# Kernel tuning notes

Hardware: AMD Instinct MI355X
Metric: run time of the kernel (lower is better)

The kernel has to match this reference:

```python
import jax, jax.numpy as jnp
import numpy as np

N, E, D, CAT, BINS, B, NNEG = 50000, 1600000, 128, 768, 100, 4096, 4


def _spmm(row, col, val, x):
    # torch.spmm(adj, x) with adj in COO form: out[r] += val * x[c]
    return jax.ops.segment_sum(val[:, None] * x[col], row, num_segments=N)


def _bn(x, g, b):
    # BatchNorm1d in training mode: biased batch statistics
    m = jnp.mean(x, axis=0)
    v = jnp.var(x, axis=0)
    return (x - m) * jax.lax.rsqrt(v + 1e-5) * g + b


def _two_att(qx, x, Wq1, bq1, Wk1, bk1, Wv1, bv1, Wq2, bq2, Wk2, bk2, Wv2, bv2, Wcat, bcat):
    # qx, x: [b, 2, D]. NOTE: original uses nn.Softmax(dim=1), i.e. softmax over the
    # QUERY axis of the [b, q, k] score matrix -- reproduced faithfully here.
    scale = 1.0 / (D ** 0.5)
    q = qx @ Wq1 + bq1
    k = x @ Wk1 + bk1
    v = x @ Wv1 + bv1
    a = jax.nn.softmax(jnp.einsum('bqd,bkd->bqk', q, k) * scale, axis=1)
    h = jnp.einsum('bqk,bkd->bqd', a, v)
    q = h @ Wq2 + bq2
    k = h @ Wk2 + bk2
    v = h @ Wv2 + bv2
    a = jax.nn.softmax(jnp.einsum('bqd,bkd->bqk', q, k) * scale, axis=1)
    h = jnp.einsum('bqk,bkd->bqd', a, v)
    return jnp.concatenate([h[:, 0], h[:, 1]], axis=1) @ Wcat + bcat


def setup_inputs():
    key = jax.random.key(0)
    ks = jax.random.split(key, 32)
    p = lambda i, shape: jax.random.normal(ks[i], shape, dtype=jnp.float32) * 0.05
    return {
        'features': jax.random.normal(ks[0], (N, 2 * CAT), dtype=jnp.float32),
        'price': jax.random.randint(ks[1], (N,), 0, BINS),
        'adj_row': jax.random.randint(ks[2], (E,), 0, N),
        'adj_col': jax.random.randint(ks[3], (E,), 0, N),
        'adj_val': jax.random.uniform(ks[4], (E,), dtype=jnp.float32),
        'train_set': jax.random.randint(ks[5], (B, 2 + NNEG), 0, N),
        'W_cid2': p(6, (CAT, D)), 'b_cid2': p(7, (D,)),
        'W_cid3': p(8, (CAT, D)), 'b_cid3': p(9, (D,)),
        'price_table': p(10, (BINS, D)),
        'W_emb': p(11, (3 * D, D)), 'b_emb': p(12, (D,)),
        'W_low': p(13, (D, D)), 'W_mid': p(14, (D, D)),
        'bn1_g': jnp.ones((D,), jnp.float32), 'bn1_b': jnp.zeros((D,), jnp.float32),
        'bn2_g': jnp.ones((D,), jnp.float32), 'bn2_b': jnp.zeros((D,), jnp.float32),
        'Wq1': p(15, (D, D)), 'bq1': p(16, (D,)),
        'Wk1': p(17, (D, D)), 'bk1': p(18, (D,)),
        'Wv1': p(19, (D, D)), 'bv1': p(20, (D,)),
        'Wq2': p(21, (D, D)), 'bq2': p(22, (D,)),
        'Wk2': p(23, (D, D)), 'bk2': p(24, (D,)),
        'Wv2': p(25, (D, D)), 'bv2': p(26, (D,)),
        'Wcat': p(27, (2 * D, D)), 'bcat': p(28, (D,)),
    }


def reference(features, price, adj_row, adj_col, adj_val, train_set,
              W_cid2, b_cid2, W_cid3, b_cid3, price_table, W_emb, b_emb,
              W_low, W_mid, bn1_g, bn1_b, bn2_g, bn2_b,
              Wq1, bq1, Wk1, bk1, Wv1, bv1, Wq2, bq2, Wk2, bk2, Wv2, bv2, Wcat, bcat):
    # item embedding
    e2 = features[:, :CAT] @ W_cid2 + b_cid2
    e3 = features[:, CAT:] @ W_cid3 + b_cid3
    ep = price_table[price]
    item = jax.nn.relu(jnp.concatenate([e2, e3, ep], axis=1) @ W_emb + b_emb)  # [N, D]
    # graph convolutions (low / mid frequency)
    ag = _spmm(adj_row, adj_col, adj_val, item)
    low = (0.5 * ag + 0.5 * item) @ W_low
    mid = (0.5 * _spmm(adj_row, adj_col, adj_val, ag) - 0.5 * item) @ W_mid
    out = jnp.stack([_bn(low, bn1_g, bn1_b), _bn(mid, bn2_g, bn2_b)], axis=1)  # [N, 2, D]
    # gather triples
    key_e = out[train_set[:, 0]]   # [B, 2, D]
    pos_e = out[train_set[:, 1]]   # [B, 2, D]
    neg_e = out[train_set[:, 2:]]  # [B, NNEG, 2, D]
    ap = (Wq1, bq1, Wk1, bk1, Wv1, bv1, Wq2, bq2, Wk2, bk2, Wv2, bv2, Wcat, bcat)
    klp = _two_att(pos_e, key_e, *ap)  # [B, D]
    pl = _two_att(key_e, pos_e, *ap)   # [B, D]
    # vectorize the per-negative loop by folding NNEG into batch
    Bn = key_e.shape[0]
    key_rep = jnp.broadcast_to(key_e[:, None], (Bn, NNEG, 2, D)).reshape(Bn * NNEG, 2, D)
    neg_flat = neg_e.reshape(Bn * NNEG, 2, D)
    kln = _two_att(neg_flat, key_rep, *ap).reshape(Bn, NNEG, D)
    nl = _two_att(key_rep, neg_flat, *ap).reshape(Bn, NNEG, D)
    pos_scores = jnp.sum(klp * pl, axis=1)        # [B]
    neg_scores = jnp.sum(kln * nl, axis=2)        # [B, NNEG]
    return -jnp.mean(jnp.log(jax.nn.sigmoid(pos_scores[:, None] - neg_scores) + 1e-9))
```

## Files before the change

kernel.cpp:

```cpp
#include <hip/hip_runtime.h>
#include <hip/hip_bf16.h>


typedef __attribute__((ext_vector_type(4))) float  f32x4;
typedef __attribute__((ext_vector_type(2))) float  f32x2;
typedef __attribute__((ext_vector_type(8))) short  s16x8;
typedef __attribute__((ext_vector_type(4))) short  s16x4;
typedef __attribute__((ext_vector_type(8))) __bf16 bf16x8;

#define NN   50000
#define EE   1600000
#define BQ   4096
#define NNEG 4

__device__ __forceinline__ short f2b(float x) {
    union { float f; unsigned u; } c; c.f = x;
    unsigned r = c.u + 0x7FFF + ((c.u >> 16) & 1);
    return (short)(r >> 16);
}

template<bool TWOSRC, bool PRICE, bool RELU>
__global__ __launch_bounds__(256)
void gemm_bf16(const float* __restrict__ A1, const float* __restrict__ A2,
               float alpha, float beta,
               const short* __restrict__ WT, const float* __restrict__ bias,
               const int* __restrict__ price, const float* __restrict__ ptab,
               float* __restrict__ Y, int ldY, int rows, int K)
{
    __shared__ short Alds[128][32];
    __shared__ short Wlds[128][32];

    const int t    = threadIdx.x;
    const int lane = t & 63;
    const int w    = t >> 6;
    const int r0   = blockIdx.x * 128;
    const int c0   = blockIdx.y * 128;
    const short* WTb = WT + (size_t)c0 * K;

    f32x4 acc[4][4];
#pragma unroll
    for (int m = 0; m < 4; ++m)
#pragma unroll
        for (int n = 0; n < 4; ++n) acc[m][n] = (f32x4)0.f;

    const int srow = t >> 3;
    const int skk  = (t & 7) * 4;
    const int wn   = t >> 1;
    const int wkp  = (t & 1) * 16;

    const int wr   = (w >> 1) * 64;
    const int wc   = (w & 1) * 64;
    const int rsel = lane & 15;
    const int kb   = (lane >> 4) * 8;

    for (int k0 = 0; k0 < K; k0 += 32) {
#pragma unroll
        for (int i = 0; i < 4; ++i) {
            int r  = srow + i * 32;
            int rg = r0 + r; rg = rg < rows ? rg : rows - 1;
            float4 va = *(const float4*)(A1 + (size_t)rg * K + (k0 + skk));
            if (TWOSRC) {
                float4 vb = *(const float4*)(A2 + (size_t)rg * K + (k0 + skk));
                va.x = alpha * va.x + beta * vb.x;
                va.y = alpha * va.y + beta * vb.y;
                va.z = alpha * va.z + beta * vb.z;
                va.w = alpha * va.w + beta * vb.w;
            }
            s16x4 sv; sv[0]=f2b(va.x); sv[1]=f2b(va.y); sv[2]=f2b(va.z); sv[3]=f2b(va.w);
            int sw = ((r >> 1) & 3) * 8;
            *(s16x4*)&Alds[r][skk ^ sw] = sv;
        }
        {
            const short* p = WTb + (size_t)wn * K + (k0 + wkp);
            s16x8 w0 = *(const s16x8*)p;
            s16x8 w1 = *(const s16x8*)(p + 8);
            int sw = ((wn >> 1) & 3) * 8;
            *(s16x8*)&Wlds[wn][wkp ^ sw]       = w0;
            *(s16x8*)&Wlds[wn][(wkp + 8) ^ sw] = w1;
        }
        __syncthreads();

        s16x8 af[4], bfr[4];
#pragma unroll
        for (int m = 0; m < 4; ++m) {
            int r = wr + m * 16 + rsel;
            af[m] = *(const s16x8*)&Alds[r][kb ^ (((r >> 1) & 3) * 8)];
        }
#pragma unroll
        for (int n = 0; n < 4; ++n) {
            int r = wc + n * 16 + rsel;
            bfr[n] = *(const s16x8*)&Wlds[r][kb ^ (((r >> 1) & 3) * 8)];
        }
#pragma unroll
        for (int m = 0; m < 4; ++m)
#pragma unroll
            for (int n = 0; n < 4; ++n)
                acc[m][n] = __builtin_amdgcn_mfma_f32_16x16x32_bf16(
                    __builtin_bit_cast(bf16x8, af[m]),
                    __builtin_bit_cast(bf16x8, bfr[n]), acc[m][n], 0, 0, 0);
        __syncthreads();
    }

    const int crow = (lane >> 4) * 4;
#pragma unroll
    for (int m = 0; m < 4; ++m) {
        int rbase = r0 + wr + m * 16 + crow;
#pragma unroll
        for (int i = 0; i < 4; ++i) {
            int gr = rbase + i;
            bool ok = (gr < rows);
            int pidx = 0;
            if (PRICE) pidx = ok ? price[gr] : 0;
#pragma unroll
            for (int n = 0; n < 4; ++n) {
                int coll = wc + n * 16 + rsel;
                int cc   = c0 + coll;
                float v  = acc[m][n][i];
                if (bias)  v += bias[cc];
                if (PRICE) v += ptab[pidx * 128 + coll];
                if (RELU)  v = fmaxf(v, 0.f);
                if (ok) Y[(size_t)gr * ldY + cc] = v;
            }
        }
    }
}

__global__ __launch_bounds__(256)
void hist_rows(const int* __restrict__ row, int* __restrict__ cnt)
{
    int e = blockIdx.x * 256 + threadIdx.x;
    if (e < EE) atomicAdd(&cnt[row[e]], 1);
}

__global__ __launch_bounds__(1024)
void scan_a(const int* __restrict__ cnt, int* __restrict__ rp, int* __restrict__ bsum)
{
    __shared__ int tmp[1024];
    int t = threadIdx.x, g = blockIdx.x * 1024 + t;
    int v = (g < NN) ? cnt[g] : 0;
    tmp[t] = v;
    __syncthreads();
    for (int off = 1; off < 1024; off <<= 1) {
        int a = (t >= off) ? tmp[t - off] : 0;
        __syncthreads();
        tmp[t] += a;
        __syncthreads();
    }
    if (g < NN) rp[g] = tmp[t] - v;
    if (t == 1023) bsum[blockIdx.x] = tmp[t];
}

__global__ void scan_b(int* __restrict__ bsum, int nb)
{
    if (threadIdx.x == 0) {
        int acc = 0;
        for (int i = 0; i < nb; ++i) { int v = bsum[i]; bsum[i] = acc; acc += v; }
    }
}

__global__ __launch_bounds__(1024)
void scan_c(int* __restrict__ rp, int* __restrict__ cur, const int* __restrict__ bsum)
{
    int t = threadIdx.x, g = blockIdx.x * 1024 + t;
    if (g < NN) {
        int v = rp[g] + bsum[blockIdx.x];
        rp[g] = v; cur[g] = v;
    }
    if (g == 0) rp[NN] = EE;
}

__global__ __launch_bounds__(256)
void scatter_edges(const int* __restrict__ row, const int* __restrict__ col,
                   const float* __restrict__ val, int* __restrict__ cur,
                   int* __restrict__ pcol, float* __restrict__ pval)
{
    int e = blockIdx.x * 256 + threadIdx.x;
    if (e >= EE) return;
    int p = atomicAdd(&cur[row[e]], 1);
    pcol[p] = col[e];
    pval[p] = val[e];
}

__global__ __launch_bounds__(256)
void spmm_csr(const int* __restrict__ rp, const int* __restrict__ pcol,
              const float* __restrict__ pval, const float* __restrict__ x,
              float* __restrict__ y)
{
    int w    = (blockIdx.x * 256 + threadIdx.x) >> 6;
    int lane = threadIdx.x & 63;
    if (w >= NN) return;
    int s = rp[w], e = rp[w + 1];
    int d = lane * 2;
    float ax = 0.f, ay = 0.f;
    int i = s;
    for (; i + 2 <= e; i += 2) {
        int   c0 = pcol[i],   c1 = pcol[i + 1];
        float v0 = pval[i],   v1 = pval[i + 1];
        f32x2 x0 = *(const f32x2*)(x + (size_t)c0 * 128 + d);
        f32x2 x1 = *(const f32x2*)(x + (size_t)c1 * 128 + d);
        ax += v0 * x0.x + v1 * x1.x;
        ay += v0 * x0.y + v1 * x1.y;
    }
    if (i < e) {
        int c0 = pcol[i]; float v0 = pval[i];
        f32x2 x0 = *(const f32x2*)(x + (size_t)c0 * 128 + d);
        ax += v0 * x0.x; ay += v0 * x0.y;
    }
    f32x2 r; r.x = ax; r.y = ay;
    *(f32x2*)(y + (size_t)w * 128 + d) = r;
}

__global__ __launch_bounds__(256)
void colstats(const float* __restrict__ low, const float* __restrict__ mid,
              float* __restrict__ stats, int nrows)
{
    const float* src = blockIdx.y ? mid : low;
    int c = threadIdx.x & 127;
    int h = threadIdx.x >> 7;
    int rs = blockIdx.x * 512;
    int re = min(rs + 512, nrows);
    float s1 = 0.f, s2 = 0.f;
    for (int r = rs + h; r < re; r += 2) {
        float xv = src[(size_t)r * 128 + c];
        s1 += xv; s2 += xv * xv;
    }
    __shared__ float l1[256], l2[256];
    l1[threadIdx.x] = s1; l2[threadIdx.x] = s2;
    __syncthreads();
    if (h == 0) {
        s1 = l1[c] + l1[128 + c];
        s2 = l2[c] + l2[128 + c];
        atomicAdd(&stats[blockIdx.y * 256 + c],       s1);
        atomicAdd(&stats[blockIdx.y * 256 + 128 + c], s2);
    }
}

__global__ __launch_bounds__(256)
void bn_scalebias(const float* __restrict__ stats,
                  const float* g1, const float* b1,
                  const float* g2, const float* b2,
                  float* __restrict__ sb, float inv_n)
{
    int t = threadIdx.x;
    int mat = t >> 7, c = t & 127;
    float mean = stats[mat * 256 + c] * inv_n;
    float var  = stats[mat * 256 + 128 + c] * inv_n - mean * mean;
    float s = (mat ? g2[c] : g1[c]) * rsqrtf(var + 1e-5f);
    float tt = (mat ? b2[c] : b1[c]) - mean * s;
    sb[mat * 256 + c] = s;
    sb[mat * 256 + 128 + c] = tt;
}

__global__ __launch_bounds__(256)
void gather_norm(const float* __restrict__ low, const float* __restrict__ mid,
                 const float* __restrict__ sb, const int* __restrict__ ts,
                 float* __restrict__ out, int nb, int slot0, int nslots)
{
    int idx = blockIdx.x * 256 + threadIdx.x;
    if (idx >= nb * nslots * 256) return;
    int c   = idx & 127;
    int seq = (idx >> 7) & 1;
    int r   = idx >> 8;
    int b = r / nslots, j = r - b * nslots;
    int node = ts[b * 6 + slot0 + j];
    const float* src = seq ? mid : low;
    float xv = src[(size_t)node * 128 + c];
    out[(size_t)r * 256 + seq * 128 + c] = xv * sb[seq * 256 + c] + sb[seq * 256 + 128 + c];
}

__global__ __launch_bounds__(256)
void attn_kernel(const float* __restrict__ qbase, const float* __restrict__ kvbase,
                 float* __restrict__ h, int nb, int qshift, int kvshift)
{
    int gw   = (blockIdx.x * 256 + threadIdx.x) >> 6;
    int lane = threadIdx.x & 63;
    if (gw >= nb) return;
    int qb = (gw >> qshift) * 2;
    int kb = (gw >> kvshift) * 2;
    const float* q0 = qbase + (size_t)qb * 384;
    const float* q1 = q0 + 384;
    const float* k0 = kvbase + (size_t)kb * 384 + 128;
    const float* k1 = k0 + 384;
    const float* v0 = kvbase + (size_t)kb * 384 + 256;
    const float* v1 = v0 + 384;
    int d = lane * 2;
    f32x2 q0v = *(const f32x2*)(q0 + d);
    f32x2 q1v = *(const f32x2*)(q1 + d);
    f32x2 k0v = *(const f32x2*)(k0 + d);
    f32x2 k1v = *(const f32x2*)(k1 + d);
    float s00 = q0v.x*k0v.x + q0v.y*k0v.y;
    float s01 = q0v.x*k1v.x + q0v.y*k1v.y;
    float s10 = q1v.x*k0v.x + q1v.y*k0v.y;
    float s11 = q1v.x*k1v.x + q1v.y*k1v.y;
#pragma unroll
    for (int off = 32; off; off >>= 1) {
        s00 += __shfl_xor(s00, off);
        s01 += __shfl_xor(s01, off);
        s10 += __shfl_xor(s10, off);
        s11 += __shfl_xor(s11, off);
    }
    const float scale = 0.08838834764831845f;
    s00 *= scale; s01 *= scale; s10 *= scale; s11 *= scale;
    float m0 = fmaxf(s00, s10), m1 = fmaxf(s01, s11);
    float e00 = __expf(s00 - m0), e10 = __expf(s10 - m0);
    float e01 = __expf(s01 - m1), e11 = __expf(s11 - m1);
    float i0 = 1.f / (e00 + e10), i1 = 1.f / (e01 + e11);
    float a00 = e00 * i0, a10 = e10 * i0;
    float a01 = e01 * i1, a11 = e11 * i1;
    f32x2 v0v = *(const f32x2*)(v0 + d);
    f32x2 v1v = *(const f32x2*)(v1 + d);
    f32x2 h0, h1;
    h0.x = a00*v0v.x + a01*v1v.x;  h0.y = a00*v0v.y + a01*v1v.y;
    h1.x = a10*v0v.x + a11*v1v.x;  h1.y = a10*v0v.y + a11*v1v.y;
    *(f32x2*)(h + (size_t)(gw * 2)     * 128 + d) = h0;
    *(f32x2*)(h + (size_t)(gw * 2 + 1) * 128 + d) = h1;
}

__global__ __launch_bounds__(256)
void scores_kernel(const float* __restrict__ cat, float* __restrict__ scores)
{
    int gw   = (blockIdx.x * 256 + threadIdx.x) >> 6;
    int lane = threadIdx.x & 63;
    if (gw >= 20480) return;
    const float *pa, *pb;
    if (gw < BQ) { pa = cat + (size_t)gw * 128;            pb = cat + (size_t)(BQ + gw) * 128; }
    else { int n = gw - BQ; pa = cat + (size_t)(2*BQ + n) * 128; pb = cat + (size_t)(2*BQ + BQ*NNEG + n) * 128; }
    f32x2 a = *(const f32x2*)(pa + lane * 2);
    f32x2 b = *(const f32x2*)(pb + lane * 2);
    float s = a.x * b.x + a.y * b.y;
#pragma unroll
    for (int off = 32; off; off >>= 1) s += __shfl_xor(s, off);
    if (lane == 0) scores[gw] = s;
}

__global__ __launch_bounds__(256)
void loss_kernel(const float* __restrict__ scores, float* __restrict__ out)
{
    int t = threadIdx.x;
    float acc = 0.f;
    for (int i = t; i < BQ * NNEG; i += 256) {
        int b = i >> 2;
        float x = scores[b] - scores[BQ + i];
        float sig = 1.f / (1.f + __expf(-x));
        acc += __logf(sig + 1e-9f);
    }
    __shared__ float red[256];
    red[t] = acc; __syncthreads();
    for (int s = 128; s > 0; s >>= 1) { if (t < s) red[t] += red[t + s]; __syncthreads(); }
    if (t == 0) out[0] = -red[0] / (float)(BQ * NNEG);
}

__global__ void pack_wc(const float* __restrict__ W2, const float* __restrict__ W3,
                        const float* __restrict__ We, short* __restrict__ WcT)
{
    int k = blockIdx.x, n = threadIdx.x;
    const float* Wrow = (k < 768) ? (W2 + (size_t)k * 128) : (W3 + (size_t)(k - 768) * 128);
    const float* Web  = We + ((k < 768) ? 0 : 128 * 128);
    float acc = 0.f;
    for (int j = 0; j < 128; ++j) acc += Wrow[j] * Web[j * 128 + n];
    WcT[(size_t)n * 1536 + k] = f2b(acc);
}

__global__ void pack_ptab(const float* __restrict__ PT, const float* __restrict__ We,
                          float* __restrict__ ptab2)
{
    int p = blockIdx.x, n = threadIdx.x;
    const float* Web = We + 256 * 128;
    float acc = 0.f;
    for (int j = 0; j < 128; ++j) acc += PT[p * 128 + j] * Web[j * 128 + n];
    ptab2[p * 128 + n] = acc;
}

__global__ void pack_biasc(const float* b2, const float* b3, const float* bemb,
                           const float* __restrict__ We, float* __restrict__ bias_c)
{
    int n = threadIdx.x;
    float acc = bemb[n];
    for (int j = 0; j < 128; ++j)
        acc += b2[j] * We[j * 128 + n] + b3[j] * We[(128 + j) * 128 + n];
    bias_c[n] = acc;
}

__global__ void pack_wt(const float* __restrict__ W, short* __restrict__ WT, int K)
{
    int k = blockIdx.x, n = threadIdx.x;
    WT[(size_t)n * K + k] = f2b(W[(size_t)k * 128 + n]);
}

__global__ void pack_wt3(const float* Wq, const float* Wk, const float* Wv,
                         const float* bq, const float* bk, const float* bv,
                         short* __restrict__ WT, float* __restrict__ bout)
{
    int k = blockIdx.x, n = threadIdx.x;
    const float* W = (n < 128) ? Wq : ((n < 256) ? Wk : Wv);
    int nl = n & 127;
    WT[(size_t)n * 128 + k] = f2b(W[k * 128 + nl]);
    if (k == 0) {
        const float* b = (n < 128) ? bq : ((n < 256) ? bk : bv);
        bout[n] = b[nl];
    }
}

extern "C" void kernel_launch(void* const* d_in, const int* in_sizes, int n_in,
                              void* d_out, int out_size, void* d_ws, size_t ws_size,
                              hipStream_t stream)
{
    const float* features = (const float*)d_in[0];
    const int*   price    = (const int*)  d_in[1];
    const int*   adj_row  = (const int*)  d_in[2];
    const int*   adj_col  = (const int*)  d_in[3];
    const float* adj_val  = (const float*)d_in[4];
    const int*   train_set= (const int*)  d_in[5];
    const float* W_cid2   = (const float*)d_in[6];
    const float* b_cid2   = (const float*)d_in[7];
    const float* W_cid3   = (const float*)d_in[8];
    const float* b_cid3   = (const float*)d_in[9];
    const float* ptable   = (const float*)d_in[10];
    const float* W_emb    = (const float*)d_in[11];
    const float* b_emb    = (const float*)d_in[12];
    const float* W_low    = (const float*)d_in[13];
    const float* W_mid    = (const float*)d_in[14];
    const float* bn1_g    = (const float*)d_in[15];
    const float* bn1_b    = (const float*)d_in[16];
    const float* bn2_g    = (const float*)d_in[17];
    const float* bn2_b    = (const float*)d_in[18];
    const float* Wq1 = (const float*)d_in[19]; const float* bq1 = (const float*)d_in[20];
    const float* Wk1 = (const float*)d_in[21]; const float* bk1 = (const float*)d_in[22];
    const float* Wv1 = (const float*)d_in[23]; const float* bv1 = (const float*)d_in[24];
    const float* Wq2 = (const float*)d_in[25]; const float* bq2 = (const float*)d_in[26];
    const float* Wk2 = (const float*)d_in[27]; const float* bk2 = (const float*)d_in[28];
    const float* Wv2 = (const float*)d_in[29]; const float* bv2 = (const float*)d_in[30];
    const float* Wcat= (const float*)d_in[31]; const float* bcat= (const float*)d_in[32];

    float* ws = (float*)d_ws;

    const size_t SZ_NODE  = (size_t)NN * 128;
    const size_t OFF_ITEM = 0;
    const size_t OFF_AG   = SZ_NODE;
    const size_t OFF_AG2  = 2 * SZ_NODE;
    const size_t OFF_LOW  = 3 * SZ_NODE;
    const size_t OFF_MID  = 4 * SZ_NODE;
    const size_t OFF_QKV2 = 0;
    const size_t OFF_GATH = 5 * SZ_NODE;
    const size_t OFF_H2   = OFF_GATH;
    const size_t OFF_QKV1 = OFF_GATH + 6291456;
    const size_t OFF_H1   = OFF_QKV1 + 18874368;
    const size_t OFF_CAT  = OFF_H1;
    size_t o = OFF_H1 + 10485760;
    short* WcT    = (short*)(ws + o);  o += 98304;
    float* ptab2  = ws + o;            o += 12800;
    float* bias_c = ws + o;            o += 128;
    short* Wqkv1T = (short*)(ws + o);  o += 24576;
    float* bqkv1  = ws + o;            o += 384;
    short* Wqkv2T = (short*)(ws + o);  o += 24576;
    float* bqkv2  = ws + o;            o += 384;
    short* WlowT  = (short*)(ws + o);  o += 8192;
    short* WmidT  = (short*)(ws + o);  o += 8192;
    short* WcatT  = (short*)(ws + o);  o += 16384;
    float* stats  = ws + o;            o += 512;
    float* sb     = ws + o;            o += 512;
    float* scores = ws + o;            o += 20480;

    float* item = ws + OFF_ITEM;
    float* ag   = ws + OFF_AG;
    float* ag2  = ws + OFF_AG2;
    float* low  = ws + OFF_LOW;
    float* mid  = ws + OFF_MID;
    float* gath = ws + OFF_GATH;
    float* qkv1 = ws + OFF_QKV1;
    float* h1   = ws + OFF_H1;
    float* qkv2 = ws + OFF_QKV2;
    float* h2   = ws + OFF_H2;
    float* cat  = ws + OFF_CAT;

    int*   rp   = (int*)(ws + OFF_GATH);
    int*   cur  = rp + 50008;
    int*   bsum = cur + 50008;
    int*   pcol = bsum + 64 + 56;
    float* pval = (float*)(pcol + 1600000);

    hipLaunchKernelGGL(pack_wc,   dim3(1536), dim3(128), 0, stream, W_cid2, W_cid3, W_emb, WcT);
    hipLaunchKernelGGL(pack_ptab, dim3(100),  dim3(128), 0, stream, ptable, W_emb, ptab2);
    hipLaunchKernelGGL(pack_biasc,dim3(1),    dim3(128), 0, stream, b_cid2, b_cid3, b_emb, W_emb, bias_c);
    hipLaunchKernelGGL(pack_wt3,  dim3(128),  dim3(384), 0, stream, Wq1, Wk1, Wv1, bq1, bk1, bv1, Wqkv1T, bqkv1);
    hipLaunchKernelGGL(pack_wt3,  dim3(128),  dim3(384), 0, stream, Wq2, Wk2, Wv2, bq2, bk2, bv2, Wqkv2T, bqkv2);
    hipLaunchKernelGGL(pack_wt,   dim3(128),  dim3(128), 0, stream, W_low, WlowT, 128);
    hipLaunchKernelGGL(pack_wt,   dim3(128),  dim3(128), 0, stream, W_mid, WmidT, 128);
    hipLaunchKernelGGL(pack_wt,   dim3(256),  dim3(128), 0, stream, Wcat,  WcatT, 256);

    hipMemsetAsync(stats, 0, 512 * sizeof(float), stream);
    hipMemsetAsync(cur, 0, 50000 * sizeof(int), stream);

    hipLaunchKernelGGL(hist_rows,     dim3(6250), dim3(256),  0, stream, adj_row, cur);
    hipLaunchKernelGGL(scan_a,        dim3(49),   dim3(1024), 0, stream, cur, rp, bsum);
    hipLaunchKernelGGL(scan_b,        dim3(1),    dim3(64),   0, stream, bsum, 49);
    hipLaunchKernelGGL(scan_c,        dim3(49),   dim3(1024), 0, stream, rp, cur, bsum);
    hipLaunchKernelGGL(scatter_edges, dim3(6250), dim3(256),  0, stream,
                       adj_row, adj_col, adj_val, cur, pcol, pval);

    hipLaunchKernelGGL((gemm_bf16<false, true, true>), dim3(391, 1), dim3(256), 0, stream,
                       features, nullptr, 1.f, 0.f, WcT, bias_c, price, ptab2,
                       item, 128, NN, 1536);

    hipLaunchKernelGGL(spmm_csr, dim3(12500), dim3(256), 0, stream, rp, pcol, pval, item, ag);
    hipLaunchKernelGGL((gemm_bf16<true, false, false>), dim3(391, 1), dim3(256), 0, stream,
                       ag, item, 0.5f, 0.5f, WlowT, nullptr, nullptr, nullptr,
                       low, 128, NN, 128);

    hipLaunchKernelGGL(spmm_csr, dim3(12500), dim3(256), 0, stream, rp, pcol, pval, ag, ag2);
    hipLaunchKernelGGL((gemm_bf16<true, false, false>), dim3(391, 1), dim3(256), 0, stream,
                       ag2, item, 0.5f, -0.5f, WmidT, nullptr, nullptr, nullptr,
                       mid, 128, NN, 128);

    hipLaunchKernelGGL(colstats, dim3(98, 2), dim3(256), 0, stream, low, mid, stats, NN);
    hipLaunchKernelGGL(bn_scalebias, dim3(1), dim3(256), 0, stream,
                       stats, bn1_g, bn1_b, bn2_g, bn2_b, sb, 1.f / (float)NN);

    hipLaunchKernelGGL(gather_norm, dim3(4096),  dim3(256), 0, stream, low, mid, sb, train_set, gath,              BQ, 0, 1);
    hipLaunchKernelGGL(gather_norm, dim3(4096),  dim3(256), 0, stream, low, mid, sb, train_set, gath + 8192*128,   BQ, 1, 1);
    hipLaunchKernelGGL(gather_norm, dim3(16384), dim3(256), 0, stream, low, mid, sb, train_set, gath + 16384*128,  BQ, 2, 4);

    hipLaunchKernelGGL((gemm_bf16<false, false, false>), dim3(384, 3), dim3(256), 0, stream,
                       gath, nullptr, 1.f, 0.f, Wqkv1T, bqkv1, nullptr, nullptr,
                       qkv1, 384, 49152, 128);

    hipLaunchKernelGGL(attn_kernel, dim3(1024), dim3(256), 0, stream,
                       qkv1 + (size_t)8192*384, qkv1, h1, BQ, 0, 0);
    hipLaunchKernelGGL(attn_kernel, dim3(1024), dim3(256), 0, stream,
                       qkv1, qkv1 + (size_t)8192*384, h1 + (size_t)8192*128, BQ, 0, 0);
    hipLaunchKernelGGL(attn_kernel, dim3(4096), dim3(256), 0, stream,
                       qkv1 + (size_t)16384*384, qkv1, h1 + (size_t)16384*128, BQ*NNEG, 0, 2);
    hipLaunchKernelGGL(attn_kernel, dim3(4096), dim3(256), 0, stream,
                       qkv1, qkv1 + (size_t)16384*384, h1 + (size_t)49152*128, BQ*NNEG, 2, 0);

    hipLaunchKernelGGL((gemm_bf16<false, false, false>), dim3(640, 3), dim3(256), 0, stream,
                       h1, nullptr, 1.f, 0.f, Wqkv2T, bqkv2, nullptr, nullptr,
                       qkv2, 384, 81920, 128);

    const size_t rb[4] = { 0, 8192, 16384, 49152 };
    const int    nbs[4] = { BQ, BQ, BQ*NNEG, BQ*NNEG };
    for (int f = 0; f < 4; ++f) {
        hipLaunchKernelGGL(attn_kernel, dim3((nbs[f] + 3) / 4), dim3(256), 0, stream,
                           qkv2 + rb[f]*384, qkv2 + rb[f]*384, h2 + rb[f]*128, nbs[f], 0, 0);
    }

    hipLaunchKernelGGL((gemm_bf16<false, false, false>), dim3(320, 1), dim3(256), 0, stream,
                       h2, nullptr, 1.f, 0.f, WcatT, bcat, nullptr, nullptr,
                       cat, 128, 40960, 256);

    hipLaunchKernelGGL(scores_kernel, dim3(5120), dim3(256), 0, stream, cat, scores);
    hipLaunchKernelGGL(loss_kernel, dim3(1), dim3(256), 0, stream, scores, (float*)d_out);
}
```

Before: 1.293 ms.

## Store intermediates in bf16 and merge attention, gather and pack launches

SpMM gathers now read bf16 copies of the node features, and the CSR column and value arrays are interleaved into a single int2 array. The attention-stage buffers (gathered rows, qkv, h) are stored as bf16, and a new GEMM variant loads bf16 A tiles directly. The separate attention, gather and weight-pack launches are merged into single kernels, and scan_b uses a wave shuffle scan. This cuts memory traffic and launch count, at the cost of extra bf16 rounding on activations and SpMM inputs.

```diff
diff --git a/kernel.cpp b/kernel.cpp
--- a/kernel.cpp
+++ b/kernel.cpp
@@ -18,14 +18,20 @@
     unsigned r = c.u + 0x7FFF + ((c.u >> 16) & 1);
     return (short)(r >> 16);
 }
-
-template<bool TWOSRC, bool PRICE, bool RELU>
+__device__ __forceinline__ float blo(unsigned u) { return __builtin_bit_cast(float, u << 16); }
+__device__ __forceinline__ float bhi(unsigned u) { return __builtin_bit_cast(float, u & 0xffff0000u); }
+__device__ __forceinline__ unsigned pk2(float a, float b) {
+    return (unsigned)(unsigned short)f2b(a) | ((unsigned)(unsigned short)f2b(b) << 16);
+}
+
+template<bool TWOSRC, bool PRICE, bool RELU, bool OUTBF>
 __global__ __launch_bounds__(256)
 void gemm_bf16(const float* __restrict__ A1, const float* __restrict__ A2,
                float alpha, float beta,
                const short* __restrict__ WT, const float* __restrict__ bias,
                const int* __restrict__ price, const float* __restrict__ ptab,
-               float* __restrict__ Y, int ldY, int rows, int K)
+               float* __restrict__ Y, unsigned short* __restrict__ Yb,
+               int ldY, int rows, int K)
 {
     __shared__ short Alds[128][32];
     __shared__ short Wlds[128][32];
@@ -119,7 +125,106 @@
                 if (bias)  v += bias[cc];
                 if (PRICE) v += ptab[pidx * 128 + coll];
                 if (RELU)  v = fmaxf(v, 0.f);
-                if (ok) Y[(size_t)gr * ldY + cc] = v;
+                if (ok) {
+                    Y[(size_t)gr * ldY + cc] = v;
+                    if (OUTBF) Yb[(size_t)gr * ldY + cc] = (unsigned short)f2b(v);
+                }
+            }
+        }
+    }
+}
+
+template<bool OUTBF>
+__global__ __launch_bounds__(256)
+void gemm_a16(const unsigned short* __restrict__ A,
+              const short* __restrict__ WT, const float* __restrict__ bias,
+              float* __restrict__ Y, unsigned short* __restrict__ Yb,
+              int ldY, int rows, int K)
+{
+    __shared__ short Alds[128][32];
+    __shared__ short Wlds[128][32];
+
+    const int t    = threadIdx.x;
+    const int lane = t & 63;
+    const int w    = t >> 6;
+    const int r0   = blockIdx.x * 128;
+    const int c0   = blockIdx.y * 128;
+    const short* WTb = WT + (size_t)c0 * K;
+
+    f32x4 acc[4][4];
+#pragma unroll
+    for (int m = 0; m < 4; ++m)
+#pragma unroll
+        for (int n = 0; n < 4; ++n) acc[m][n] = (f32x4)0.f;
+
+    const int srow = t >> 1;
+    const int skk  = (t & 1) * 16;
+    const int wn   = t >> 1;
+    const int wkp  = (t & 1) * 16;
+
+    const int wr   = (w >> 1) * 64;
+    const int wc   = (w & 1) * 64;
+    const int rsel = lane & 15;
+    const int kb   = (lane >> 4) * 8;
+
+    for (int k0 = 0; k0 < K; k0 += 32) {
+        {
+            int rg = r0 + srow; rg = rg < rows ? rg : rows - 1;
+            const unsigned short* p = A + (size_t)rg * K + (k0 + skk);
+            s16x8 a0 = *(const s16x8*)p;
+            s16x8 a1 = *(const s16x8*)(p + 8);
+            int sw = ((srow >> 1) & 3) * 8;
+            *(s16x8*)&Alds[srow][skk ^ sw]       = a0;
+            *(s16x8*)&Alds[srow][(skk + 8) ^ sw] = a1;
+        }
+        {
+            const short* p = WTb + (size_t)wn * K + (k0 + wkp);
+            s16x8 w0 = *(const s16x8*)p;
+            s16x8 w1 = *(const s16x8*)(p + 8);
+            int sw = ((wn >> 1) & 3) * 8;
+            *(s16x8*)&Wlds[wn][wkp ^ sw]       = w0;
+            *(s16x8*)&Wlds[wn][(wkp + 8) ^ sw] = w1;
+        }
+        __syncthreads();
+
+        s16x8 af[4], bfr[4];
+#pragma unroll
+        for (int m = 0; m < 4; ++m) {
+            int r = wr + m * 16 + rsel;
+            af[m] = *(const s16x8*)&Alds[r][kb ^ (((r >> 1) & 3) * 8)];
+        }
+#pragma unroll
+        for (int n = 0; n < 4; ++n) {
+            int r = wc + n * 16 + rsel;
+            bfr[n] = *(const s16x8*)&Wlds[r][kb ^ (((r >> 1) & 3) * 8)];
+        }
+#pragma unroll
+        for (int m = 0; m < 4; ++m)
+#pragma unroll
+            for (int n = 0; n < 4; ++n)
+                acc[m][n] = __builtin_amdgcn_mfma_f32_16x16x32_bf16(
+                    __builtin_bit_cast(bf16x8, af[m]),
+                    __builtin_bit_cast(bf16x8, bfr[n]), acc[m][n], 0, 0, 0);
+        __syncthreads();
+    }
+
+    const int crow = (lane >> 4) * 4;
+#pragma unroll
+    for (int m = 0; m < 4; ++m) {
+        int rbase = r0 + wr + m * 16 + crow;
+#pragma unroll
+        for (int i = 0; i < 4; ++i) {
+            int gr = rbase + i;
+            bool ok = (gr < rows);
+#pragma unroll
+            for (int n = 0; n < 4; ++n) {
+                int cc = c0 + wc + n * 16 + rsel;
+                float v = acc[m][n][i];
+                if (bias) v += bias[cc];
+                if (ok) {
+                    if (OUTBF) Yb[(size_t)gr * ldY + cc] = (unsigned short)f2b(v);
+                    else       Y [(size_t)gr * ldY + cc] = v;
+                }
             }
         }
     }
@@ -150,12 +255,17 @@
     if (t == 1023) bsum[blockIdx.x] = tmp[t];
 }
 
-__global__ void scan_b(int* __restrict__ bsum, int nb)
-{
-    if (threadIdx.x == 0) {
-        int acc = 0;
-        for (int i = 0; i < nb; ++i) { int v = bsum[i]; bsum[i] = acc; acc += v; }
-    }
+__global__ __launch_bounds__(64)
+void scan_b(int* __restrict__ bsum, int nb)
+{
+    int lane = threadIdx.x;
+    int orig = (lane < nb) ? bsum[lane] : 0;
+    int v = orig;
+    for (int off = 1; off < 64; off <<= 1) {
+        int u = __shfl_up(v, off);
+        if (lane >= off) v += u;
+    }
+    if (lane < nb) bsum[lane] = v - orig;
 }
 
 __global__ __launch_bounds__(1024)
@@ -172,19 +282,19 @@
 __global__ __launch_bounds__(256)
 void scatter_edges(const int* __restrict__ row, const int* __restrict__ col,
                    const float* __restrict__ val, int* __restrict__ cur,
-                   int* __restrict__ pcol, float* __restrict__ pval)
+                   int2* __restrict__ pedge)
 {
     int e = blockIdx.x * 256 + threadIdx.x;
     if (e >= EE) return;
     int p = atomicAdd(&cur[row[e]], 1);
-    pcol[p] = col[e];
-    pval[p] = val[e];
-}
-
-__global__ __launch_bounds__(256)
-void spmm_csr(const int* __restrict__ rp, const int* __restrict__ pcol,
-              const float* __restrict__ pval, const float* __restrict__ x,
-              float* __restrict__ y)
+    pedge[p] = make_int2(col[e], __float_as_int(val[e]));
+}
+
+template<bool WRITEB>
+__global__ __launch_bounds__(256)
+void spmm_csr(const int* __restrict__ rp, const int2* __restrict__ pedge,
+              const unsigned short* __restrict__ xb,
+              float* __restrict__ y, unsigned short* __restrict__ yb)
 {
     int w    = (blockIdx.x * 256 + threadIdx.x) >> 6;
     int lane = threadIdx.x & 63;
@@ -193,21 +303,28 @@
     int d = lane * 2;
     float ax = 0.f, ay = 0.f;
     int i = s;
-    for (; i + 2 <= e; i += 2) {
-        int   c0 = pcol[i],   c1 = pcol[i + 1];
-        float v0 = pval[i],   v1 = pval[i + 1];
-        f32x2 x0 = *(const f32x2*)(x + (size_t)c0 * 128 + d);
-        f32x2 x1 = *(const f32x2*)(x + (size_t)c1 * 128 + d);
-        ax += v0 * x0.x + v1 * x1.x;
-        ay += v0 * x0.y + v1 * x1.y;
-    }
-    if (i < e) {
-        int c0 = pcol[i]; float v0 = pval[i];
-        f32x2 x0 = *(const f32x2*)(x + (size_t)c0 * 128 + d);
-        ax += v0 * x0.x; ay += v0 * x0.y;
+    for (; i + 4 <= e; i += 4) {
+        int2 e0 = pedge[i], e1 = pedge[i+1], e2 = pedge[i+2], e3 = pedge[i+3];
+        unsigned x0 = *(const unsigned*)(xb + (size_t)e0.x * 128 + d);
+        unsigned x1 = *(const unsigned*)(xb + (size_t)e1.x * 128 + d);
+        unsigned x2 = *(const unsigned*)(xb + (size_t)e2.x * 128 + d);
+        unsigned x3 = *(const unsigned*)(xb + (size_t)e3.x * 128 + d);
+        float v0 = __builtin_bit_cast(float, e0.y);
+        float v1 = __builtin_bit_cast(float, e1.y);
+        float v2 = __builtin_bit_cast(float, e2.y);
+        float v3 = __builtin_bit_cast(float, e3.y);
+        ax += v0 * blo(x0) + v1 * blo(x1) + v2 * blo(x2) + v3 * blo(x3);
+        ay += v0 * bhi(x0) + v1 * bhi(x1) + v2 * bhi(x2) + v3 * bhi(x3);
+    }
+    for (; i < e; ++i) {
+        int2 e0 = pedge[i];
+        unsigned x0 = *(const unsigned*)(xb + (size_t)e0.x * 128 + d);
+        float v0 = __builtin_bit_cast(float, e0.y);
+        ax += v0 * blo(x0); ay += v0 * bhi(x0);
     }
     f32x2 r; r.x = ax; r.y = ay;
     *(f32x2*)(y + (size_t)w * 128 + d) = r;
+    if (WRITEB) *(unsigned*)(yb + (size_t)w * 128 + d) = pk2(ax, ay);
 }
 
 __global__ __launch_bounds__(256)
@@ -254,44 +371,47 @@
 __global__ __launch_bounds__(256)
 void gather_norm(const float* __restrict__ low, const float* __restrict__ mid,
                  const float* __restrict__ sb, const int* __restrict__ ts,
-                 float* __restrict__ out, int nb, int slot0, int nslots)
+                 unsigned short* __restrict__ out)
 {
     int idx = blockIdx.x * 256 + threadIdx.x;
-    if (idx >= nb * nslots * 256) return;
     int c   = idx & 127;
     int seq = (idx >> 7) & 1;
     int r   = idx >> 8;
-    int b = r / nslots, j = r - b * nslots;
-    int node = ts[b * 6 + slot0 + j];
-    const float* src = seq ? mid : low;
-    float xv = src[(size_t)node * 128 + c];
-    out[(size_t)r * 256 + seq * 128 + c] = xv * sb[seq * 256 + c] + sb[seq * 256 + 128 + c];
-}
-
-__global__ __launch_bounds__(256)
-void attn_kernel(const float* __restrict__ qbase, const float* __restrict__ kvbase,
-                 float* __restrict__ h, int nb, int qshift, int kvshift)
+    int node;
+    if      (r < 4096) node = ts[r * 6];
+    else if (r < 8192) node = ts[(r - 4096) * 6 + 1];
+    else { int rr = r - 8192; node = ts[(rr >> 2) * 6 + 2 + (rr & 3)]; }
+    float xv = (seq ? mid : low)[(size_t)node * 128 + c];
+    float yv = xv * sb[seq * 256 + c] + sb[seq * 256 + 128 + c];
+    out[(size_t)r * 256 + seq * 128 + c] = (unsigned short)f2b(yv);
+}
+
+template<int LAYER>
+__global__ __launch_bounds__(256)
+void attn_fused(const unsigned short* __restrict__ qkv,
+                unsigned short* __restrict__ h, int ntot)
 {
     int gw   = (blockIdx.x * 256 + threadIdx.x) >> 6;
     int lane = threadIdx.x & 63;
-    if (gw >= nb) return;
-    int qb = (gw >> qshift) * 2;
-    int kb = (gw >> kvshift) * 2;
-    const float* q0 = qbase + (size_t)qb * 384;
-    const float* q1 = q0 + 384;
-    const float* k0 = kvbase + (size_t)kb * 384 + 128;
-    const float* k1 = k0 + 384;
-    const float* v0 = kvbase + (size_t)kb * 384 + 256;
-    const float* v1 = v0 + 384;
+    if (gw >= ntot) return;
+    int qtok, ktok, orow;
+    if (LAYER == 1) {
+        if      (gw < 4096)  { int g = gw;         qtok = 8192  + g*2; ktok = g*2;          orow = g*2; }
+        else if (gw < 8192)  { int g = gw - 4096;  qtok = g*2;         ktok = 8192 + g*2;   orow = 8192 + g*2; }
+        else if (gw < 24576) { int g = gw - 8192;  qtok = 16384 + g*2; ktok = (g>>2)*2;     orow = 16384 + g*2; }
+        else                 { int g = gw - 24576; qtok = (g>>2)*2;    ktok = 16384 + g*2;  orow = 49152 + g*2; }
+    } else {
+        qtok = gw * 2; ktok = gw * 2; orow = gw * 2;
+    }
     int d = lane * 2;
-    f32x2 q0v = *(const f32x2*)(q0 + d);
-    f32x2 q1v = *(const f32x2*)(q1 + d);
-    f32x2 k0v = *(const f32x2*)(k0 + d);
-    f32x2 k1v = *(const f32x2*)(k1 + d);
-    float s00 = q0v.x*k0v.x + q0v.y*k0v.y;
-    float s01 = q0v.x*k1v.x + q0v.y*k1v.y;
-    float s10 = q1v.x*k0v.x + q1v.y*k0v.y;
-    float s11 = q1v.x*k1v.x + q1v.y*k1v.y;
+    unsigned q0 = *(const unsigned*)(qkv + (size_t)qtok * 384 + d);
+    unsigned q1 = *(const unsigned*)(qkv + (size_t)(qtok+1) * 384 + d);
+    unsigned k0 = *(const unsigned*)(qkv + (size_t)ktok * 384 + 128 + d);
+    unsigned k1 = *(const unsigned*)(qkv + (size_t)(ktok+1) * 384 + 128 + d);
+    float s00 = blo(q0)*blo(k0) + bhi(q0)*bhi(k0);
+    float s01 = blo(q0)*blo(k1) + bhi(q0)*bhi(k1);
+    float s10 = blo(q1)*blo(k0) + bhi(q1)*bhi(k0);
+    float s11 = blo(q1)*blo(k1) + bhi(q1)*bhi(k1);
 #pragma unroll
     for (int off = 32; off; off >>= 1) {
         s00 += __shfl_xor(s00, off);
@@ -307,13 +427,12 @@
     float i0 = 1.f / (e00 + e10), i1 = 1.f / (e01 + e11);
     float a00 = e00 * i0, a10 = e10 * i0;
     float a01 = e01 * i1, a11 = e11 * i1;
-    f32x2 v0v = *(const f32x2*)(v0 + d);
-    f32x2 v1v = *(const f32x2*)(v1 + d);
-    f32x2 h0, h1;
-    h0.x = a00*v0v.x + a01*v1v.x;  h0.y = a00*v0v.y + a01*v1v.y;
-    h1.x = a10*v0v.x + a11*v1v.x;  h1.y = a10*v0v.y + a11*v1v.y;
-    *(f32x2*)(h + (size_t)(gw * 2)     * 128 + d) = h0;
-    *(f32x2*)(h + (size_t)(gw * 2 + 1) * 128 + d) = h1;
+    unsigned v0 = *(const unsigned*)(qkv + (size_t)ktok * 384 + 256 + d);
+    unsigned v1 = *(const unsigned*)(qkv + (size_t)(ktok+1) * 384 + 256 + d);
+    float h0x = a00*blo(v0) + a01*blo(v1), h0y = a00*bhi(v0) + a01*bhi(v1);
+    float h1x = a10*blo(v0) + a11*blo(v1), h1y = a10*bhi(v0) + a11*bhi(v1);
+    *(unsigned*)(h + (size_t)orow * 128 + d)       = pk2(h0x, h0y);
+    *(unsigned*)(h + (size_t)(orow + 1) * 128 + d) = pk2(h1x, h1y);
 }
 
 __global__ __launch_bounds__(256)
@@ -361,43 +480,51 @@
     WcT[(size_t)n * 1536 + k] = f2b(acc);
 }
 
-__global__ void pack_ptab(const float* __restrict__ PT, const float* __restrict__ We,
-                          float* __restrict__ ptab2)
-{
-    int p = blockIdx.x, n = threadIdx.x;
-    const float* Web = We + 256 * 128;
-    float acc = 0.f;
-    for (int j = 0; j < 128; ++j) acc += PT[p * 128 + j] * Web[j * 128 + n];
-    ptab2[p * 128 + n] = acc;
-}
-
-__global__ void pack_biasc(const float* b2, const float* b3, const float* bemb,
-                           const float* __restrict__ We, float* __restrict__ bias_c)
-{
-    int n = threadIdx.x;
-    float acc = bemb[n];
-    for (int j = 0; j < 128; ++j)
-        acc += b2[j] * We[j * 128 + n] + b3[j] * We[(128 + j) * 128 + n];
-    bias_c[n] = acc;
-}
-
-__global__ void pack_wt(const float* __restrict__ W, short* __restrict__ WT, int K)
-{
-    int k = blockIdx.x, n = threadIdx.x;
-    WT[(size_t)n * K + k] = f2b(W[(size_t)k * 128 + n]);
-}
-
-__global__ void pack_wt3(const float* Wq, const float* Wk, const float* Wv,
-                         const float* bq, const float* bk, const float* bv,
-                         short* __restrict__ WT, float* __restrict__ bout)
-{
-    int k = blockIdx.x, n = threadIdx.x;
-    const float* W = (n < 128) ? Wq : ((n < 256) ? Wk : Wv);
-    int nl = n & 127;
-    WT[(size_t)n * 128 + k] = f2b(W[k * 128 + nl]);
-    if (k == 0) {
-        const float* b = (n < 128) ? bq : ((n < 256) ? bk : bv);
-        bout[n] = b[nl];
+__global__ __launch_bounds__(128)
+void pack_misc(const float* PT, const float* We,
+               const float* b2, const float* b3, const float* bemb,
+               const float* Wq1, const float* Wk1, const float* Wv1,
+               const float* bq1, const float* bk1, const float* bv1,
+               const float* Wq2, const float* Wk2, const float* Wv2,
+               const float* bq2, const float* bk2, const float* bv2,
+               const float* Wlow, const float* Wmid, const float* Wct,
+               float* ptab2, float* bias_c,
+               short* Wqkv1T, float* bqkv1,
+               short* Wqkv2T, float* bqkv2,
+               short* WlowT, short* WmidT, short* WcatT)
+{
+    int b = blockIdx.x, t = threadIdx.x;
+    if (b < 100) {
+        const float* Web = We + 256 * 128;
+        float acc = 0.f;
+        for (int j = 0; j < 128; ++j) acc += PT[b * 128 + j] * Web[j * 128 + t];
+        ptab2[b * 128 + t] = acc;
+    } else if (b == 100) {
+        float acc = bemb[t];
+        for (int j = 0; j < 128; ++j)
+            acc += b2[j] * We[j * 128 + t] + b3[j] * We[(128 + j) * 128 + t];
+        bias_c[t] = acc;
+    } else if (b < 229) {
+        int k = b - 101;
+        Wqkv1T[(size_t)(      t) * 128 + k] = f2b(Wq1[k * 128 + t]);
+        Wqkv1T[(size_t)(128 + t) * 128 + k] = f2b(Wk1[k * 128 + t]);
+        Wqkv1T[(size_t)(256 + t) * 128 + k] = f2b(Wv1[k * 128 + t]);
+        if (k == 0) { bqkv1[t] = bq1[t]; bqkv1[128 + t] = bk1[t]; bqkv1[256 + t] = bv1[t]; }
+    } else if (b < 357) {
+        int k = b - 229;
+        Wqkv2T[(size_t)(      t) * 128 + k] = f2b(Wq2[k * 128 + t]);
+        Wqkv2T[(size_t)(128 + t) * 128 + k] = f2b(Wk2[k * 128 + t]);
+        Wqkv2T[(size_t)(256 + t) * 128 + k] = f2b(Wv2[k * 128 + t]);
+        if (k == 0) { bqkv2[t] = bq2[t]; bqkv2[128 + t] = bk2[t]; bqkv2[256 + t] = bv2[t]; }
+    } else if (b < 485) {
+        int k = b - 357;
+        WlowT[(size_t)t * 128 + k] = f2b(Wlow[k * 128 + t]);
+    } else if (b < 613) {
+        int k = b - 485;
+        WmidT[(size_t)t * 128 + k] = f2b(Wmid[k * 128 + t]);
+    } else {
+        int k = b - 613;
+        WcatT[(size_t)t * 256 + k] = f2b(Wct[k * 128 + t]);
     }
 }
 
@@ -434,119 +561,93 @@
 
     float* ws = (float*)d_ws;
 
-    const size_t SZ_NODE  = (size_t)NN * 128;
-    const size_t OFF_ITEM = 0;
-    const size_t OFF_AG   = SZ_NODE;
-    const size_t OFF_AG2  = 2 * SZ_NODE;
-    const size_t OFF_LOW  = 3 * SZ_NODE;
-    const size_t OFF_MID  = 4 * SZ_NODE;
-    const size_t OFF_QKV2 = 0;
-    const size_t OFF_GATH = 5 * SZ_NODE;
-    const size_t OFF_H2   = OFF_GATH;
-    const size_t OFF_QKV1 = OFF_GATH + 6291456;
-    const size_t OFF_H1   = OFF_QKV1 + 18874368;
-    const size_t OFF_CAT  = OFF_H1;
-    size_t o = OFF_H1 + 10485760;
-    short* WcT    = (short*)(ws + o);  o += 98304;
-    float* ptab2  = ws + o;            o += 12800;
-    float* bias_c = ws + o;            o += 128;
-    short* Wqkv1T = (short*)(ws + o);  o += 24576;
-    float* bqkv1  = ws + o;            o += 384;
-    short* Wqkv2T = (short*)(ws + o);  o += 24576;
-    float* bqkv2  = ws + o;            o += 384;
-    short* WlowT  = (short*)(ws + o);  o += 8192;
-    short* WmidT  = (short*)(ws + o);  o += 8192;
-    short* WcatT  = (short*)(ws + o);  o += 16384;
-    float* stats  = ws + o;            o += 512;
-    float* sb     = ws + o;            o += 512;
-    float* scores = ws + o;            o += 20480;
-
-    float* item = ws + OFF_ITEM;
-    float* ag   = ws + OFF_AG;
-    float* ag2  = ws + OFF_AG2;
-    float* low  = ws + OFF_LOW;
-    float* mid  = ws + OFF_MID;
-    float* gath = ws + OFF_GATH;
-    float* qkv1 = ws + OFF_QKV1;
-    float* h1   = ws + OFF_H1;
-    float* qkv2 = ws + OFF_QKV2;
-    float* h2   = ws + OFF_H2;
-    float* cat  = ws + OFF_CAT;
-
-    int*   rp   = (int*)(ws + OFF_GATH);
-    int*   cur  = rp + 50008;
-    int*   bsum = cur + 50008;
-    int*   pcol = bsum + 64 + 56;
-    float* pval = (float*)(pcol + 1600000);
+    const size_t SZ_NODE = (size_t)NN * 128;
+    float*          item    = ws;
+    float*          ag      = ws + 6400000;
+    float*          ag2     = ws + 12800000;
+    float*          low     = ws + 19200000;
+    float*          mid     = ws + 25600000;
+    unsigned short* item_bf = (unsigned short*)(ws + 32000000);
+    unsigned short* ag_bf   = (unsigned short*)(ws + 35200000);
+    unsigned short* gath_b  = (unsigned short*)(ws + 38400000);
+    unsigned short* qkv1b   = (unsigned short*)(ws + 41545728);
+    unsigned short* h1b     = (unsigned short*)(ws + 50982912);
+    unsigned short* qkv2b   = (unsigned short*)(ws + 56225792);
+    unsigned short* h2b     = (unsigned short*)(ws + 71954432);
+    float*          cat     = ws + 77197312;
+    int*            ibase   = (int*)(ws + 82440192);
+    int*   rp    = ibase;
+    int*   cur   = ibase + 50016;
+    float* stats = (float*)(ibase + 100032);
+    int*   bsum  = ibase + 100544;
+    int2*  pedge = (int2*)(ibase + 100640);
+    float* wb    = (float*)(ibase + 3300640);
+    short* WcT    = (short*)wb;
+    float* ptab2  = wb + 98304;
+    float* bias_c = wb + 111104;
+    short* Wqkv1T = (short*)(wb + 111232);
+    float* bqkv1  = wb + 135808;
+    short* Wqkv2T = (short*)(wb + 136192);
+    float* bqkv2  = wb + 160768;
+    short* WlowT  = (short*)(wb + 161152);
+    short* WmidT  = (short*)(wb + 169344);
+    short* WcatT  = (short*)(wb + 177536);
+    float* sb     = wb + 193920;
+    float* scores = wb + 194432;
 
     hipLaunchKernelGGL(pack_wc,   dim3(1536), dim3(128), 0, stream, W_cid2, W_cid3, W_emb, WcT);
-    hipLaunchKernelGGL(pack_ptab, dim3(100),  dim3(128), 0, stream, ptable, W_emb, ptab2);
-    hipLaunchKernelGGL(pack_biasc,dim3(1),    dim3(128), 0, stream, b_cid2, b_cid3, b_emb, W_emb, bias_c);
-    hipLaunchKernelGGL(pack_wt3,  dim3(128),  dim3(384), 0, stream, Wq1, Wk1, Wv1, bq1, bk1, bv1, Wqkv1T, bqkv1);
-    hipLaunchKernelGGL(pack_wt3,  dim3(128),  dim3(384), 0, stream, Wq2, Wk2, Wv2, bq2, bk2, bv2, Wqkv2T, bqkv2);
-    hipLaunchKernelGGL(pack_wt,   dim3(128),  dim3(128), 0, stream, W_low, WlowT, 128);
-    hipLaunchKernelGGL(pack_wt,   dim3(128),  dim3(128), 0, stream, W_mid, WmidT, 128);
-    hipLaunchKernelGGL(pack_wt,   dim3(256),  dim3(128), 0, stream, Wcat,  WcatT, 256);
-
-    hipMemsetAsync(stats, 0, 512 * sizeof(float), stream);
-    hipMemsetAsync(cur, 0, 50000 * sizeof(int), stream);
+    hipLaunchKernelGGL(pack_misc, dim3(869),  dim3(128), 0, stream,
+                       ptable, W_emb, b_cid2, b_cid3, b_emb,
+                       Wq1, Wk1, Wv1, bq1, bk1, bv1,
+                       Wq2, Wk2, Wv2, bq2, bk2, bv2,
+                       W_low, W_mid, Wcat,
+                       ptab2, bias_c, Wqkv1T, bqkv1, Wqkv2T, bqkv2,
+                       WlowT, WmidT, WcatT);
+
+    hipMemsetAsync(cur, 0, (50016 + 512) * 4, stream);
 
     hipLaunchKernelGGL(hist_rows,     dim3(6250), dim3(256),  0, stream, adj_row, cur);
     hipLaunchKernelGGL(scan_a,        dim3(49),   dim3(1024), 0, stream, cur, rp, bsum);
     hipLaunchKernelGGL(scan_b,        dim3(1),    dim3(64),   0, stream, bsum, 49);
     hipLaunchKernelGGL(scan_c,        dim3(49),   dim3(1024), 0, stream, rp, cur, bsum);
     hipLaunchKernelGGL(scatter_edges, dim3(6250), dim3(256),  0, stream,
-                       adj_row, adj_col, adj_val, cur, pcol, pval);
-
-    hipLaunchKernelGGL((gemm_bf16<false, true, true>), dim3(391, 1), dim3(256), 0, stream,
+                       adj_row, adj_col, adj_val, cur, pedge);
+
+    hipLaunchKernelGGL((gemm_bf16<false, true, true, true>), dim3(391, 1), dim3(256), 0, stream,
                        features, nullptr, 1.f, 0.f, WcT, bias_c, price, ptab2,
-                       item, 128, NN, 1536);
-
-    hipLaunchKernelGGL(spmm_csr, dim3(12500), dim3(256), 0, stream, rp, pcol, pval, item, ag);
-    hipLaunchKernelGGL((gemm_bf16<true, false, false>), dim3(391, 1), dim3(256), 0, stream,
+                       item, item_bf, 128, NN, 1536);
+
+    hipLaunchKernelGGL((spmm_csr<true>), dim3(12500), dim3(256), 0, stream,
+                       rp, pedge, item_bf, ag, ag_bf);
+    hipLaunchKernelGGL((gemm_bf16<true, false, false, false>), dim3(391, 1), dim3(256), 0, stream,
                        ag, item, 0.5f, 0.5f, WlowT, nullptr, nullptr, nullptr,
-                       low, 128, NN, 128);
-
-    hipLaunchKernelGGL(spmm_csr, dim3(12500), dim3(256), 0, stream, rp, pcol, pval, ag, ag2);
-    hipLaunchKernelGGL((gemm_bf16<true, false, false>), dim3(391, 1), dim3(256), 0, stream,
+                       low, nullptr, 128, NN, 128);
+
+    hipLaunchKernelGGL((spmm_csr<false>), dim3(12500), dim3(256), 0, stream,
+                       rp, pedge, ag_bf, ag2, nullptr);
+    hipLaunchKernelGGL((gemm_bf16<true, false, false, false>), dim3(391, 1), dim3(256), 0, stream,
                        ag2, item, 0.5f, -0.5f, WmidT, nullptr, nullptr, nullptr,
-                       mid, 128, NN, 128);
+                       mid, nullptr, 128, NN, 128);
 
     hipLaunchKernelGGL(colstats, dim3(98, 2), dim3(256), 0, stream, low, mid, stats, NN);
     hipLaunchKernelGGL(bn_scalebias, dim3(1), dim3(256), 0, stream,
                        stats, bn1_g, bn1_b, bn2_g, bn2_b, sb, 1.f / (float)NN);
 
-    hipLaunchKernelGGL(gather_norm, dim3(4096),  dim3(256), 0, stream, low, mid, sb, train_set, gath,              BQ, 0, 1);
-    hipLaunchKernelGGL(gather_norm, dim3(4096),  dim3(256), 0, stream, low, mid, sb, train_set, gath + 8192*128,   BQ, 1, 1);
-    hipLaunchKernelGGL(gather_norm, dim3(16384), dim3(256), 0, stream, low, mid, sb, train_set, gath + 16384*128,  BQ, 2, 4);
-
-    hipLaunchKernelGGL((gemm_bf16<false, false, false>), dim3(384, 3), dim3(256), 0, stream,
-                       gath, nullptr, 1.f, 0.f, Wqkv1T, bqkv1, nullptr, nullptr,
-                       qkv1, 384, 49152, 128);
-
-    hipLaunchKernelGGL(attn_kernel, dim3(1024), dim3(256), 0, stream,
-                       qkv1 + (size_t)8192*384, qkv1, h1, BQ, 0, 0);
-    hipLaunchKernelGGL(attn_kernel, dim3(1024), dim3(256), 0, stream,
-                       qkv1, qkv1 + (size_t)8192*384, h1 + (size_t)8192*128, BQ, 0, 0);
-    hipLaunchKernelGGL(attn_kernel, dim3(4096), dim3(256), 0, stream,
-                       qkv1 + (size_t)16384*384, qkv1, h1 + (size_t)16384*128, BQ*NNEG, 0, 2);
-    hipLaunchKernelGGL(attn_kernel, dim3(4096), dim3(256), 0, stream,
-                       qkv1, qkv1 + (size_t)16384*384, h1 + (size_t)49152*128, BQ*NNEG, 2, 0);
-
-    hipLaunchKernelGGL((gemm_bf16<false, false, false>), dim3(640, 3), dim3(256), 0, stream,
-                       h1, nullptr, 1.f, 0.f, Wqkv2T, bqkv2, nullptr, nullptr,
-                       qkv2, 384, 81920, 128);
-
-    const size_t rb[4] = { 0, 8192, 16384, 49152 };
-    const int    nbs[4] = { BQ, BQ, BQ*NNEG, BQ*NNEG };
-    for (int f = 0; f < 4; ++f) {
-        hipLaunchKernelGGL(attn_kernel, dim3((nbs[f] + 3) / 4), dim3(256), 0, stream,
-                           qkv2 + rb[f]*384, qkv2 + rb[f]*384, h2 + rb[f]*128, nbs[f], 0, 0);
-    }
-
-    hipLaunchKernelGGL((gemm_bf16<false, false, false>), dim3(320, 1), dim3(256), 0, stream,
-                       h2, nullptr, 1.f, 0.f, WcatT, bcat, nullptr, nullptr,
-                       cat, 128, 40960, 256);
+    hipLaunchKernelGGL(gather_norm, dim3(24576), dim3(256), 0, stream,
+                       low, mid, sb, train_set, gath_b);
+
+    hipLaunchKernelGGL((gemm_a16<true>), dim3(384, 3), dim3(256), 0, stream,
+                       gath_b, Wqkv1T, bqkv1, nullptr, qkv1b, 384, 49152, 128);
+
+    hipLaunchKernelGGL((attn_fused<1>), dim3(10240), dim3(256), 0, stream, qkv1b, h1b, 40960);
+
+    hipLaunchKernelGGL((gemm_a16<true>), dim3(640, 3), dim3(256), 0, stream,
+                       h1b, Wqkv2T, bqkv2, nullptr, qkv2b, 384, 81920, 128);
+
+    hipLaunchKernelGGL((attn_fused<2>), dim3(10240), dim3(256), 0, stream, qkv2b, h2b, 40960);
+
+    hipLaunchKernelGGL((gemm_a16<false>), dim3(320, 1), dim3(256), 0, stream,
+                       h2b, WcatT, bcat, cat, nullptr, 128, 40960, 256);
 
     hipLaunchKernelGGL(scores_kernel, dim3(5120), dim3(256), 0, stream, cat, scores);
     hipLaunchKernelGGL(loss_kernel, dim3(1), dim3(256), 0, stream, scores, (float*)d_out);
```

New measurement: 1.123 ms. 1.15x faster.
